# Kernel optimization log

Hardware: AMD Instinct MI355X
Metric: run time of the kernel (lower is better)

Reference implementation:

```python
import jax, jax.numpy as jnp
import numpy as np


def _relative_index(ih: int, iw: int) -> np.ndarray:
    # Static precompute mirroring the torch buffer.
    yy, xx = np.meshgrid(np.arange(ih), np.arange(iw), indexing='ij')
    coords = np.stack([yy.ravel(), xx.ravel()])                 # [2, n]
    rel = coords[:, :, None] - coords[:, None, :]               # [2, n, n]
    rel[0] += ih - 1
    rel[1] += iw - 1
    rel[0] *= 2 * iw - 1
    return rel.sum(0).ravel()                                   # [n*n]


def setup_inputs() -> dict:
    key = jax.random.key(0)
    ks = jax.random.split(key, 5)
    B, N, INP, OUP, HEADS = 64, 256, 512, 512, 16
    ih = iw = 16
    return {
        'x': jax.random.normal(ks[0], (B, N, INP), jnp.float32),
        'w_qkv': jax.random.normal(ks[1], (INP, 3 * OUP), jnp.float32) * 0.02,
        'rel_bias_table': jax.random.normal(ks[2], ((2 * ih - 1) * (2 * iw - 1), HEADS), jnp.float32) * 0.02,
        'w_out': jax.random.normal(ks[3], (OUP, OUP), jnp.float32) * 0.02,
        'b_out': jax.random.normal(ks[4], (OUP,), jnp.float32) * 0.02,
        'ih': ih,
        'iw': iw,
    }


def reference(x, w_qkv, rel_bias_table, w_out, b_out, ih, iw):
    B, N, _ = x.shape
    heads = rel_bias_table.shape[1]
    oup = w_out.shape[0]
    dim_head = oup // heads
    scale = dim_head ** -0.5

    qkv = jnp.einsum('bni,ij->bnj', x, w_qkv)                   # [B, N, 3*oup]
    q, k, v = jnp.split(qkv, 3, axis=-1)
    split_heads = lambda t: t.reshape(B, N, heads, dim_head).transpose(0, 2, 1, 3)
    q, k, v = split_heads(q), split_heads(k), split_heads(v)    # [B, H, N, D]

    dots = jnp.einsum('bhnd,bhmd->bhnm', q, k) * scale          # [B, H, N, N]
    rel_idx = jnp.asarray(_relative_index(int(ih), int(iw)))    # [N*N]
    bias = rel_bias_table[rel_idx].reshape(N, N, heads)         # gather
    dots = dots + bias.transpose(2, 0, 1)[None]                 # [1, H, N, N]

    attn = jax.nn.softmax(dots, axis=-1)
    out = jnp.einsum('bhnm,bhmd->bhnd', attn, v)                # [B, H, N, D]
    out = out.transpose(0, 2, 1, 3).reshape(B, N, oup)
    return jnp.einsum('bno,op->bnp', out, w_out.T) + b_out
```

## Files before the change

kernel.cpp:

```cpp
#include <hip/hip_runtime.h>
#include <stdint.h>

typedef unsigned short u16;
typedef unsigned int u32;
typedef __attribute__((ext_vector_type(8))) __bf16 bf16x8;
typedef __attribute__((ext_vector_type(2))) u32 u32x2;
typedef __attribute__((ext_vector_type(4))) u32 u32x4;
typedef __attribute__((ext_vector_type(4))) float f32x4;

__device__ __forceinline__ float bf2f(u16 x) { return __uint_as_float(((u32)x) << 16); }
__device__ __forceinline__ u16 f2bf(float f) {
  u32 u = __float_as_uint(f);
  u32 r = (u + 0x7fffu + ((u >> 16) & 1u)) >> 16;
  return (u16)r;
}
__device__ __forceinline__ u16 cvbf(float f) {
  union { __bf16 b; u16 u; } x;
  x.b = (__bf16)f;
  return x.u;
}

__device__ __forceinline__ u32x2 ld8(const u16* p) { return *(const u32x2*)p; }
__device__ __forceinline__ u32x4 ld16(const u16* p) { return *(const u32x4*)p; }
__device__ __forceinline__ bf16x8 mk_frag(u32x2 lo, u32x2 hi) {
  union { bf16x8 v; u32x2 u[2]; } t;
  t.u[0] = lo; t.u[1] = hi;
  return t.v;
}

__device__ __forceinline__ void g2l16(const void* g, void* l) {
  __builtin_amdgcn_global_load_lds(
      (const __attribute__((address_space(1))) u32*)g,
      (__attribute__((address_space(3))) u32*)l, 16, 0, 0);
}

__device__ __forceinline__ void stage_fm(u16* lds, int ch, u32x4 v) {
  int row = ch >> 2, q = ch & 3;
  *(u32x4*)&lds[(row >> 4) * 512 + q * 128 + (row & 15) * 8] = v;
}

__device__ __forceinline__ bf16x8 frag_fm(const u16* lds, int subtile, int g, int c) {
  union { bf16x8 v; u32x4 u; } t;
  t.u = ld16(&lds[subtile * 512 + g * 128 + c * 8]);
  return t.v;
}

__device__ __forceinline__ void swz_bn_bm(int& bn, int& bm) {
  const u32 nx = gridDim.x, ny = gridDim.y;
  if ((ny & 7u) == 0u) {
    u32 d = blockIdx.y * nx + blockIdx.x;
    u32 xcd = d & 7u, wi = d >> 3;
    bm = (int)(xcd * (ny >> 3) + wi / nx);
    bn = (int)(wi % nx);
  } else {
    bn = blockIdx.x;
    bm = blockIdx.y;
  }
}

__global__ void probe_dtype(const u32* __restrict__ x, u32* __restrict__ flag) {
  if (threadIdx.x == 0 && blockIdx.x == 0) {
    int cnt = 0;
    for (int i = 0; i < 32; ++i) {
      u32 e = (x[i] >> 7) & 0xffu;
      cnt += (e >= 96u && e <= 140u) ? 1 : 0;
    }
    *flag = (cnt == 32) ? 1u : 0u;
  }
}

__global__ __launch_bounds__(256) void conv4(const void* __restrict__ src, u16* __restrict__ dst,
                                             const u32* __restrict__ flag, int n4) {
  const bool isbf = (*flag != 0u);
  const int stride = gridDim.x * 256;
  for (int i = blockIdx.x * 256 + threadIdx.x; i < n4; i += stride) {
    if (isbf) {
      ((u32x2*)dst)[i] = ((const u32x2*)src)[i];
    } else {
      const float* s = (const float*)src + (size_t)i * 4;
      u32x2 o;
      o.x = (u32)f2bf(s[0]) | ((u32)f2bf(s[1]) << 16);
      o.y = (u32)f2bf(s[2]) | ((u32)f2bf(s[3]) << 16);
      ((u32x2*)dst)[i] = o;
    }
  }
}

__global__ __launch_bounds__(256) void bias_prep(const void* __restrict__ table,
                                                 float* __restrict__ biasT,
                                                 const u32* __restrict__ flag) {
  const bool isbf = (*flag != 0u);
  int i = blockIdx.x * 256 + threadIdx.x;
  if (i < 16 * 961) {
    int h = i / 961, idx = i - h * 961;
    float v = isbf ? bf2f(((const u16*)table)[idx * 16 + h])
                   : ((const float*)table)[idx * 16 + h];
    biasT[i] = v * 1.4426950408889634f;
  }
}

__global__ __launch_bounds__(256) void transpose_dt(const void* __restrict__ in,
                                                    u16* __restrict__ out,
                                                    const u32* __restrict__ flag, int R, int C) {
  __shared__ u16 t[32][33];
  const bool isbf = (*flag != 0u);
  int r0 = blockIdx.y * 32, c0 = blockIdx.x * 32;
  int rr = threadIdx.x >> 5, cc = threadIdx.x & 31;
#pragma unroll
  for (int i = 0; i < 4; ++i) {
    size_t idx = (size_t)(r0 + rr + i * 8) * C + c0 + cc;
    t[rr + i * 8][cc] = isbf ? ((const u16*)in)[idx] : f2bf(((const float*)in)[idx]);
  }
  __syncthreads();
#pragma unroll
  for (int i = 0; i < 4; ++i) out[(size_t)(c0 + rr + i * 8) * R + r0 + cc] = t[cc][rr + i * 8];
}

template <bool BIAS>
__global__ __launch_bounds__(256) void gemm_k512(const u16* __restrict__ A,
                                                 const u16* __restrict__ BT,
                                                 const u16* __restrict__ bias,
                                                 void* __restrict__ O, int ldo, int row0g,
                                                 const u32* __restrict__ flag) {
  constexpr int K = 512;
  constexpr int NT = 16;
  __shared__ u16 As[3][128 * 32];
  __shared__ u16 Bs[3][128 * 32];
  const int tid = threadIdx.x;
  const int wave = tid >> 6, lane = tid & 63;
  const int c = lane & 15, g = lane >> 4;
  const int wm = wave >> 1, wn = wave & 1;
  int bn, bm;
  swz_bn_bm(bn, bm);

  const u16* Ab = A + (size_t)bm * 128 * K;
  const u16* Bb = BT + (size_t)bn * 128 * K;

  const u16* Arow = Ab + (size_t)(wave * 16 + c) * K + 8 * g;
  const u16* Brow = Bb + (size_t)(wave * 16 + c) * K + 8 * g;
  const int ldst = wave * 512 + lane * 8;

#define STAGE_G(buf, k0)                                \
  do {                                                  \
    g2l16(Arow + (k0), &As[buf][ldst]);                 \
    g2l16(Arow + 64 * K + (k0), &As[buf][2048 + ldst]); \
    g2l16(Brow + (k0), &Bs[buf][ldst]);                 \
    g2l16(Brow + 64 * K + (k0), &Bs[buf][2048 + ldst]); \
  } while (0)

  f32x4 acc[4][4] = {};

  STAGE_G(0, 0);
  STAGE_G(1, 32);

#pragma unroll
  for (int t = 0; t < NT; ++t) {
    if (t + 1 < NT) {
      asm volatile("s_waitcnt vmcnt(4)" ::: "memory");
    } else {
      asm volatile("s_waitcnt vmcnt(0)" ::: "memory");
    }
    __builtin_amdgcn_s_barrier();
    __builtin_amdgcn_sched_barrier(0);
    if (t + 2 < NT) STAGE_G((t + 2) % 3, (t + 2) * 32);
    const u16* Ac = &As[t % 3][0];
    const u16* Bc = &Bs[t % 3][0];
    bf16x8 af[4], bfr[4];
#pragma unroll
    for (int i = 0; i < 4; ++i) {
      af[i] = frag_fm(Ac, wm * 4 + i, g, c);
      bfr[i] = frag_fm(Bc, wn * 4 + i, g, c);
    }
#pragma unroll
    for (int i = 0; i < 4; ++i)
#pragma unroll
      for (int j = 0; j < 4; ++j)
        acc[i][j] = __builtin_amdgcn_mfma_f32_16x16x32_bf16(af[i], bfr[j], acc[i][j], 0, 0, 0);
  }
#undef STAGE_G

  const bool isbf = BIAS ? (*flag != 0u) : true;
#pragma unroll
  for (int i = 0; i < 4; ++i)
#pragma unroll
    for (int j = 0; j < 4; ++j) {
      int jg = bn * 128 + wn * 64 + j * 16 + c;
      float bv = BIAS ? bf2f(bias[jg]) : 0.0f;
#pragma unroll
      for (int r = 0; r < 4; ++r) {
        int mg = bm * 128 + wm * 64 + i * 16 + 4 * g + r;
        float v = acc[i][j][r] + bv;
        size_t off = (size_t)(row0g + mg) * ldo + jg;
        if (BIAS) {
          if (isbf) ((u16*)O)[off] = f2bf(v);
          else ((float*)O)[off] = v;
        } else {
          ((u16*)O)[off] = f2bf(v);
        }
      }
    }
}

__global__ __launch_bounds__(256) void attn_kernel(const u16* __restrict__ qkv,
                                                   const float* __restrict__ biasT,
                                                   u16* __restrict__ Out) {
  __shared__ u16 smem[18432];
  float* biasS = (float*)&smem[16384];

  const int tid = threadIdx.x;
  const int wave = tid >> 6, lane = tid & 63;
  const int c = lane & 15, g = lane >> 4;
  const int half = blockIdx.x & 1;
  const int h = (blockIdx.x >> 1) & 15;
  const int b = blockIdx.x >> 5;

  const u16* xb = qkv + (size_t)b * 256 * 1536;

  u32x4 kvr[4];
#pragma unroll
  for (int i = 0; i < 4; ++i) {
    int ch = tid + i * 256;
    int m = ch >> 2;
    kvr[i] = ld16(xb + (size_t)m * 1536 + 512 + h * 32 + (ch & 3) * 8);
  }
#pragma unroll
  for (int i = 0; i < 4; ++i) stage_fm(smem, tid + i * 256, kvr[i]);

#pragma unroll
  for (int i = 0; i < 16; ++i) {
    int e2 = tid + i * 256;
    int n = e2 >> 4, d = (e2 & 15) * 2;
    u32 val = *(const u32*)(xb + (size_t)n * 1536 + 1024 + h * 32 + d);
    smem[8192 + d * 256 + (n ^ (8 * (d & 7)))] = (u16)(val & 0xffffu);
    smem[8192 + (d + 1) * 256 + (n ^ (8 * ((d + 1) & 7)))] = (u16)(val >> 16);
  }
  for (int i = tid; i < 961; i += 256) biasS[i] = biasT[h * 961 + i];

  u32x4 qv[2];
#pragma unroll
  for (int rg = 0; rg < 2; ++rg) {
    const u16* qp = xb + (size_t)((half * 2 + rg) * 64 + wave * 16 + c) * 1536 + h * 32 + 8 * g;
    qv[rg] = ld16(qp);
  }
  __syncthreads();

  const u16* Vt = &smem[8192];
  const int va = 8 * (c & 7);
  const float scale2 = 0.25503484f;
  const float* bp0 = biasS + wave * 31 + c + 12 - 4 * g;

#pragma unroll
  for (int rg = 0; rg < 2; ++rg) {
    const int rgg = half * 2 + rg;
    union { bf16x8 v; u32x4 u; } qt;
    qt.u = qv[rg];
    bf16x8 qf = qt.v;

    f32x4 o0 = {0.f, 0.f, 0.f, 0.f}, o1 = {0.f, 0.f, 0.f, 0.f};
    float smm = 0.f;

#pragma unroll
    for (int ph = 0; ph < 2; ++ph) {
      f32x4 s[8];
#pragma unroll
      for (int f = 0; f < 8; ++f) {
        bf16x8 kf = frag_fm(smem, ph * 8 + f, g, c);
        f32x4 z = {0.f, 0.f, 0.f, 0.f};
        s[f] = __builtin_amdgcn_mfma_f32_16x16x32_bf16(kf, qf, z, 0, 0, 0);
      }

      float u[8];
#pragma unroll
      for (int f = 0; f < 8; ++f) {
        const int fg = ph * 8 + f;
#pragma unroll
        for (int j = 0; j < 4; ++j) {
          float bv = bp0[(rgg * 4 - fg + 15) * 31 + 3 - j];
          s[f][j] = __builtin_amdgcn_exp2f(s[f][j] * scale2 + bv);
        }
        u[f] = (s[f][0] + s[f][1]) + (s[f][2] + s[f][3]);
      }
      smm += ((u[0] + u[4]) + (u[1] + u[5])) + ((u[2] + u[6]) + (u[3] + u[7]));

#pragma unroll
      for (int q = 0; q < 4; ++q) {
        bf16x8 pf;
        pf[0] = (__bf16)s[2 * q][0]; pf[1] = (__bf16)s[2 * q][1];
        pf[2] = (__bf16)s[2 * q][2]; pf[3] = (__bf16)s[2 * q][3];
        pf[4] = (__bf16)s[2 * q + 1][0]; pf[5] = (__bf16)s[2 * q + 1][1];
        pf[6] = (__bf16)s[2 * q + 1][2]; pf[7] = (__bf16)s[2 * q + 1][3];
        const int kg = (ph * 4 + q) * 32;
        bf16x8 v0 = mk_frag(ld8(&Vt[c * 256 + ((kg + 4 * g) ^ va)]),
                            ld8(&Vt[c * 256 + ((kg + 16 + 4 * g) ^ va)]));
        bf16x8 v1 = mk_frag(ld8(&Vt[(16 + c) * 256 + ((kg + 4 * g) ^ va)]),
                            ld8(&Vt[(16 + c) * 256 + ((kg + 16 + 4 * g) ^ va)]));
        o0 = __builtin_amdgcn_mfma_f32_16x16x32_bf16(pf, v0, o0, 0, 0, 0);
        o1 = __builtin_amdgcn_mfma_f32_16x16x32_bf16(pf, v1, o1, 0, 0, 0);
      }
    }

    smm += __shfl_xor(smm, 16, 64);
    smm += __shfl_xor(smm, 32, 64);
    const float invc = __builtin_amdgcn_rcpf(smm);

    const int nb = rgg * 64 + wave * 16 + 4 * g;
#pragma unroll
    for (int j = 0; j < 4; ++j) {
      int n = nb + j;
      size_t off = ((size_t)b * 256 + n) * 512 + h * 32;
      Out[off + c] = cvbf(o0[j] * invc);
      Out[off + 16 + c] = cvbf(o1[j] * invc);
    }
  }
}

extern "C" void kernel_launch(void* const* d_in, const int* in_sizes, int n_in, void* d_out,
                              int out_size, void* d_ws, size_t ws_size, hipStream_t stream) {
  (void)in_sizes; (void)n_in; (void)out_size;
  const void* x = d_in[0];
  const void* w_qkv = d_in[1];
  const void* table = d_in[2];
  const void* w_out = d_in[3];
  const void* b_out = d_in[4];

  char* ws = (char*)d_ws;
  u32* flag = (u32*)ws;
  u16* xc = (u16*)(ws + 256);
  u16* wqkvT = (u16*)(ws + 16777472);
  float* biasT = (float*)(ws + 18350336);
  u16* woC = (u16*)(ws + 18411840);
  u16* bC = (u16*)(ws + 18936128);
  const size_t DYN = 18937344;
  int CB = 64;
  while (CB > 1 && DYN + (size_t)CB * 1048576 > ws_size) CB >>= 1;
  u16* qkv = (u16*)(ws + DYN);
  u16* att = (u16*)(ws + DYN + (size_t)CB * 786432);

  dim3 blk(256);
  probe_dtype<<<dim3(1), dim3(64), 0, stream>>>((const u32*)x, flag);
  conv4<<<dim3(2048), blk, 0, stream>>>(x, xc, flag, 2097152);
  conv4<<<dim3(256), blk, 0, stream>>>(w_out, woC, flag, 65536);
  conv4<<<dim3(1), blk, 0, stream>>>(b_out, bC, flag, 128);
  bias_prep<<<dim3(61), blk, 0, stream>>>(table, biasT, flag);
  transpose_dt<<<dim3(48, 16), blk, 0, stream>>>(w_qkv, wqkvT, flag, 512, 1536);

  for (int s0 = 0; s0 < 64; s0 += CB) {
    const u16* xcc = xc + (size_t)s0 * 256 * 512;
    gemm_k512<false><<<dim3(12, CB * 2), blk, 0, stream>>>(xcc, wqkvT, nullptr, qkv, 1536, 0,
                                                           flag);
    attn_kernel<<<dim3(CB * 32), blk, 0, stream>>>(qkv, biasT, att);
    gemm_k512<true><<<dim3(4, CB * 2), blk, 0, stream>>>(att, woC, bC, d_out, 512, s0 * 256,
                                                         flag);
  }
}
```

Baseline: 147.9 us.

## Replace triple-buffered direct-to-LDS loads with register-staged single-buffer GEMM pipeline

The K=512 GEMM kernel stops using global_load_lds into a three-deep LDS ring. Each thread now prefetches the next K-slice into registers, stores it into a single LDS buffer, and synchronises with barriers before the MFMA fragment reads. LDS usage drops, which may help occupancy. In exchange there are two barriers per iteration, extra VGPR pressure, and less overlap between global loads and compute.

```diff
diff --git a/kernel.cpp b/kernel.cpp
--- a/kernel.cpp
+++ b/kernel.cpp
@@ -26,12 +26,6 @@
   union { bf16x8 v; u32x2 u[2]; } t;
   t.u[0] = lo; t.u[1] = hi;
   return t.v;
-}
-
-__device__ __forceinline__ void g2l16(const void* g, void* l) {
-  __builtin_amdgcn_global_load_lds(
-      (const __attribute__((address_space(1))) u32*)g,
-      (__attribute__((address_space(3))) u32*)l, 16, 0, 0);
 }
 
 __device__ __forceinline__ void stage_fm(u16* lds, int ch, u32x4 v) {
@@ -124,8 +118,8 @@
                                                  const u32* __restrict__ flag) {
   constexpr int K = 512;
   constexpr int NT = 16;
-  __shared__ u16 As[3][128 * 32];
-  __shared__ u16 Bs[3][128 * 32];
+  __shared__ u16 As[128 * 32];
+  __shared__ u16 Bs[128 * 32];
   const int tid = threadIdx.x;
   const int wave = tid >> 6, lane = tid & 63;
   const int c = lane & 15, g = lane >> 4;
@@ -136,40 +130,43 @@
   const u16* Ab = A + (size_t)bm * 128 * K;
   const u16* Bb = BT + (size_t)bn * 128 * K;
 
-  const u16* Arow = Ab + (size_t)(wave * 16 + c) * K + 8 * g;
-  const u16* Brow = Bb + (size_t)(wave * 16 + c) * K + 8 * g;
-  const int ldst = wave * 512 + lane * 8;
-
-#define STAGE_G(buf, k0)                                \
-  do {                                                  \
-    g2l16(Arow + (k0), &As[buf][ldst]);                 \
-    g2l16(Arow + 64 * K + (k0), &As[buf][2048 + ldst]); \
-    g2l16(Brow + (k0), &Bs[buf][ldst]);                 \
-    g2l16(Brow + 64 * K + (k0), &Bs[buf][2048 + ldst]); \
-  } while (0)
+  const int row0 = tid >> 2, q0 = tid & 3;
+  const u16* Asrc0 = Ab + (size_t)row0 * K + q0 * 8;
+  const u16* Bsrc0 = Bb + (size_t)row0 * K + q0 * 8;
+  const u16* Asrc1 = Asrc0 + (size_t)64 * K;
+  const u16* Bsrc1 = Bsrc0 + (size_t)64 * K;
 
   f32x4 acc[4][4] = {};
 
-  STAGE_G(0, 0);
-  STAGE_G(1, 32);
+  u32x4 a0 = ld16(Asrc0), b0 = ld16(Bsrc0), a1 = ld16(Asrc1), b1 = ld16(Bsrc1);
 
 #pragma unroll
   for (int t = 0; t < NT; ++t) {
+    if (t > 0) {
+      asm volatile("s_waitcnt lgkmcnt(0)" ::: "memory");
+      __builtin_amdgcn_s_barrier();
+      __builtin_amdgcn_sched_barrier(0);
+    }
+    stage_fm(As, tid, a0);
+    stage_fm(Bs, tid, b0);
+    stage_fm(As, tid + 256, a1);
+    stage_fm(Bs, tid + 256, b1);
     if (t + 1 < NT) {
-      asm volatile("s_waitcnt vmcnt(4)" ::: "memory");
-    } else {
-      asm volatile("s_waitcnt vmcnt(0)" ::: "memory");
-    }
+      const int k0 = (t + 1) * 32;
+      a0 = ld16(Asrc0 + k0);
+      b0 = ld16(Bsrc0 + k0);
+      a1 = ld16(Asrc1 + k0);
+      b1 = ld16(Bsrc1 + k0);
+    }
+    asm volatile("s_waitcnt lgkmcnt(0)" ::: "memory");
     __builtin_amdgcn_s_barrier();
     __builtin_amdgcn_sched_barrier(0);
-    if (t + 2 < NT) STAGE_G((t + 2) % 3, (t + 2) * 32);
-    const u16* Ac = &As[t % 3][0];
-    const u16* Bc = &Bs[t % 3][0];
+
     bf16x8 af[4], bfr[4];
 #pragma unroll
     for (int i = 0; i < 4; ++i) {
-      af[i] = frag_fm(Ac, wm * 4 + i, g, c);
-      bfr[i] = frag_fm(Bc, wn * 4 + i, g, c);
+      af[i] = frag_fm(As, wm * 4 + i, g, c);
+      bfr[i] = frag_fm(Bs, wn * 4 + i, g, c);
     }
 #pragma unroll
     for (int i = 0; i < 4; ++i)
@@ -177,7 +174,6 @@
       for (int j = 0; j < 4; ++j)
         acc[i][j] = __builtin_amdgcn_mfma_f32_16x16x32_bf16(af[i], bfr[j], acc[i][j], 0, 0, 0);
   }
-#undef STAGE_G
 
   const bool isbf = BIAS ? (*flag != 0u) : true;
 #pragma unroll
```

Result: faster. 130.1 us (-12.0%).
